# Kernel tuning notes

Hardware: AMD Instinct MI355X
Metric: run time of the kernel (lower is better)

The kernel has to match this reference:

```python
import jax, jax.numpy as jnp
import numpy as np

INF = jnp.float32(1e9)  # sentinel; true costs are O(10)


def _hungarian_cost(cost):
    """Exact min-cost perfect matching total cost (Jonker-Volgenant potentials
    algorithm, O(n^3)), matching scipy.optimize.linear_sum_assignment.
    cost: (n, n) float32 -> scalar sum of matched costs."""
    n = cost.shape[0]
    # pad with dummy row/col 0 (1-indexed algorithm)
    a = jnp.zeros((n + 1, n + 1), cost.dtype).at[1:, 1:].set(cost)

    def row_step(carry, i):
        u, v, p = carry  # u,v: dual potentials; p[j] = row matched to col j
        p = p.at[0].set(i)
        minv = jnp.full(n + 1, INF, cost.dtype)
        used = jnp.zeros(n + 1, bool)
        way = jnp.zeros(n + 1, jnp.int32)

        def cond(st):
            u, v, p, minv, used, way, j0, first = st
            return first | (p[j0] != 0)

        def body(st):
            u, v, p, minv, used, way, j0, _ = st
            used = used.at[j0].set(True)
            i0 = p[j0]
            cur = a[i0] - u[i0] - v                      # reduced costs of row i0
            upd = (~used) & (cur < minv)
            way = jnp.where(upd, j0, way)
            minv = jnp.where(upd, cur, minv)
            masked = jnp.where(used, INF, minv)
            j1 = jnp.argmin(masked).astype(jnp.int32)
            delta = masked[j1]
            # u[p[j]] += delta for used j (unused scatter adds 0, harmless)
            u = u.at[p].add(jnp.where(used, delta, 0.0))
            v = jnp.where(used, v - delta, v)
            minv = jnp.where(used, minv, minv - delta)
            return (u, v, p, minv, used, way, j1, False)

        u, v, p, minv, used, way, j0, _ = jax.lax.while_loop(
            cond, body, (u, v, p, minv, used, way, jnp.int32(0), True))

        # augment along alternating path
        def aug_body(st):
            p, j0 = st
            j1 = way[j0]
            return p.at[j0].set(p[j1]), j1

        p, _ = jax.lax.while_loop(lambda st: st[1] != 0, aug_body, (p, j0))
        return (u, v, p), None

    init = (jnp.zeros(n + 1, cost.dtype),
            jnp.zeros(n + 1, cost.dtype),
            jnp.zeros(n + 1, jnp.int32))
    (u, v, p), _ = jax.lax.scan(row_step, init,
                                jnp.arange(1, n + 1, dtype=jnp.int32))
    cols = jnp.arange(1, n + 1)
    return a[p[1:], cols].sum()


def setup_inputs() -> dict:
    key = jax.random.key(0)
    k1, k2 = jax.random.split(key)
    B, N = 8, 1024
    S1 = jax.random.normal(k1, (B, N, 3), dtype=jnp.float32)
    S2 = jax.random.normal(k2, (B, N, 3), dtype=jnp.float32)
    return {"S1": S1, "S2": S2}


def reference(S1, S2):
    B, N, _ = S1.shape
    # torch.cdist(p=2): per-sample pairwise Euclidean distances -> (B, N, N)
    diff = S1[:, :, None, :] - S2[:, None, :, :]
    cost = jnp.sqrt(jnp.sum(diff * diff, axis=-1))
    per_sample = jax.vmap(_hungarian_cost)(cost) / N  # optimal assignment cost / N
    return jnp.mean(per_sample)
```

## Files before the change

### kernel.cpp

```cpp
#include <hip/hip_runtime.h>
#include <hip/hip_fp16.h>
#include <math.h>


#define N     1024
#define BATCH 8
#define NSLOT 16
#define INFV  1e9f
#define AUC_ROUNDS 24

__global__ void emd_zero_kernel(float* out) { out[0] = 0.0f; }

__global__ __launch_bounds__(256)
void emd_dist_kernel(const float* __restrict__ S1, const float* __restrict__ S2,
                     __half* __restrict__ D) {
    int b = blockIdx.x >> 10;
    int r = blockIdx.x & (N - 1);
    const float* s1 = S1 + ((size_t)b * N + r) * 3;
    float x1 = s1[0], y1 = s1[1], z1 = s1[2];
    const float* s2 = S2 + (size_t)b * N * 3;
    __half* drow = D + ((size_t)b * N + r) * (size_t)N;
    for (int c = threadIdx.x; c < N; c += 256) {
        float dx = x1 - s2[3 * c], dy = y1 - s2[3 * c + 1], dz = z1 - s2[3 * c + 2];
        drow[c] = __float2half_rn(sqrtf(dx * dx + dy * dy + dz * dz));
    }
}

__global__ __launch_bounds__(256)
void emd_colmin_kernel(const __half* __restrict__ D, float* __restrict__ V,
                       int* __restrict__ I) {
    int b = blockIdx.x >> 2;
    int c = ((blockIdx.x & 3) << 8) + threadIdx.x;
    const __half* Db = D + ((size_t)b << 20);
    float best = INFV; int bi = 1;
    for (int r = 0; r < N; ++r) {
        float d = __half2float(Db[(size_t)r * N + c]);
        if (d < best) { best = d; bi = r + 1; }
    }
    V[b * N + c] = best;
    I[b * N + c] = bi;
}

template<int CTRL>
__device__ __forceinline__ float dppmin(float x) {
    int xi = __float_as_int(x);
    int yi = __builtin_amdgcn_update_dpp(xi, xi, CTRL, 0xF, 0xF, false);
    return fminf(x, __int_as_float(yi));
}

__device__ __forceinline__ float wave_min_f32(float x) {
    x = dppmin<0x111>(x);
    x = dppmin<0x112>(x);
    x = dppmin<0x114>(x);
    x = dppmin<0x118>(x);
    x = dppmin<0x142>(x);
    x = dppmin<0x143>(x);
    return __int_as_float(__builtin_amdgcn_readlane(__float_as_int(x), 63));
}

__global__ __launch_bounds__(1024, 1)
void emd_auction_kernel(const __half* __restrict__ Dc,
                        const float* __restrict__ Vin,
                        const int* __restrict__ Iin,
                        float* __restrict__ Vw, float* __restrict__ Uw,
                        int* __restrict__ Cw, int* __restrict__ Rw) {
    __shared__ float v0[N];
    __shared__ int   rowm[N + 1];
    __shared__ int   colm[N + 1];
    __shared__ unsigned long long bid[N + 1];
    __shared__ int   qbuf[N];
    __shared__ int   qn;

    const int tid  = threadIdx.x;
    const int lane = tid & 63;
    const int wv   = tid >> 6;
    const int b    = blockIdx.x;
    const __half* Db = Dc + ((size_t)b << 20);

    for (int t = tid; t <= N; t += 1024) { rowm[t] = 0; colm[t] = 0; bid[t] = 0ull; }
    for (int c = tid; c < N; c += 1024) v0[c] = Vin[b * N + c];
    __syncthreads();

    for (int c = tid; c < N; c += 1024) {
        int r = Iin[b * N + c];
        int old = atomicCAS(&rowm[r], 0, c + 1);
        if (old == 0) colm[c + 1] = r;
    }
    __syncthreads();

    auto rowRed16 = [&](int i, float (&red)[16]) {
        const uint4* dr = (const uint4*)(Db + (size_t)(i - 1) * N);
        uint4 w0 = dr[lane * 2 + 0];
        uint4 w1 = dr[lane * 2 + 1];
        unsigned wb[8] = { w0.x, w0.y, w0.z, w0.w, w1.x, w1.y, w1.z, w1.w };
        const float4* vp = (const float4*)(v0 + lane * 16);
        float4 vv0 = vp[0], vv1 = vp[1], vv2 = vp[2], vv3 = vp[3];
        float vv[16] = { vv0.x, vv0.y, vv0.z, vv0.w, vv1.x, vv1.y, vv1.z, vv1.w,
                         vv2.x, vv2.y, vv2.z, vv2.w, vv3.x, vv3.y, vv3.z, vv3.w };
#pragma unroll
        for (int t = 0; t < 8; ++t) {
            __half2 hh = *reinterpret_cast<const __half2*>(&wb[t]);
            float2 f2 = __half22float2(hh);
            red[2 * t]     = f2.x - vv[2 * t];
            red[2 * t + 1] = f2.y - vv[2 * t + 1];
        }
    };

    for (int round = 0; round < AUC_ROUNDS; ++round) {
        if (tid == 0) qn = 0;
        __syncthreads();
        for (int i = tid + 1; i <= N; i += 1024)
            if (rowm[i] == 0) { int p = atomicAdd(&qn, 1); qbuf[p] = i; }
        __syncthreads();
        int nq = qn;
        if (nq == 0) break;

        for (int q = wv; q < nq; q += 16) {
            int i = qbuf[q];
            float red[16];
            rowRed16(i, red);
            float a1 = INFV, a2 = INFV; int ac = 0;
            float e1 = INFV, e2 = INFV; int ec = 0;
            float f1 = INFV, f2 = INFV; int fc = 0;
            float g1 = INFV, g2 = INFV; int gc = 0;
#pragma unroll
            for (int k = 0; k < 4; ++k) {
                float u0 = red[k];
                bool t0 = u0 < a1;
                a2 = t0 ? a1 : (u0 < a2 ? u0 : a2);
                ac = t0 ? (lane * 16 + k) : ac;  a1 = t0 ? u0 : a1;
                float u1 = red[k + 4];
                bool t1 = u1 < e1;
                e2 = t1 ? e1 : (u1 < e2 ? u1 : e2);
                ec = t1 ? (lane * 16 + k + 4) : ec;  e1 = t1 ? u1 : e1;
                float u2 = red[k + 8];
                bool t2 = u2 < f1;
                f2 = t2 ? f1 : (u2 < f2 ? u2 : f2);
                fc = t2 ? (lane * 16 + k + 8) : fc;  f1 = t2 ? u2 : f1;
                float u3 = red[k + 12];
                bool t3 = u3 < g1;
                g2 = t3 ? g1 : (u3 < g2 ? u3 : g2);
                gc = t3 ? (lane * 16 + k + 12) : gc;  g1 = t3 ? u3 : g1;
            }
            bool sae = e1 < a1;
            float ae1 = sae ? e1 : a1; int aec = sae ? ec : ac;
            float ae2 = fminf(fminf(a2, e2), sae ? a1 : e1);
            bool sfg = g1 < f1;
            float fg1 = sfg ? g1 : f1; int fgc = sfg ? gc : fc;
            float fg2 = fminf(fminf(f2, g2), sfg ? f1 : g1);
            bool sall = fg1 < ae1;
            float m1 = sall ? fg1 : ae1;
            int   c1 = sall ? fgc : aec;
            float m2 = fminf(fminf(ae2, fg2), sall ? ae1 : fg1);

            float gm1 = wave_min_f32(m1);
            unsigned long long wbm = __ballot(m1 == gm1);
            int wl = __ffsll((long long)wbm) - 1;
            float cand2 = (lane == wl) ? m2 : m1;
            float gm2 = wave_min_f32(cand2);
            int gcol = __builtin_amdgcn_readlane(c1, wl);
            float inc = gm2 - gm1;

            if (lane == 0) {
                unsigned long long key =
                    ((unsigned long long)__float_as_uint(inc) << 32) |
                    (unsigned long long)(unsigned)i;
                atomicMax(&bid[gcol + 1], key);
            }
        }
        __syncthreads();

        for (int j = tid + 1; j <= N; j += 1024) {
            unsigned long long bb = bid[j];
            if (bb != 0ull) {
                bid[j] = 0ull;
                int i = (int)(unsigned)(bb & 0xFFFFFFFFull);
                float inc = __uint_as_float((unsigned)(bb >> 32));
                int old = colm[j];
                colm[j] = i;
                rowm[i] = j;
                if (old) rowm[old] = 0;
                v0[j - 1] -= inc;
            }
        }
        __syncthreads();
    }

    for (int q = wv; q < N; q += 16) {
        int i = q + 1;
        float red[16];
        rowRed16(i, red);
        int j = rowm[i];
        float rloc = red[0];
        int lo = 0, kk = 0;
        if (j) {
            lo = (j - 1) >> 4; kk = (j - 1) & 15;
#pragma unroll
            for (int k = 1; k < 16; ++k) if (k == kk) rloc = red[k];
        }
#pragma unroll
        for (int s = 1; s < 16; s <<= 1) {
#pragma unroll
            for (int k = 0; k < 16; k += 2 * s)
                red[k] = fminf(red[k], red[k + s]);
        }
        float m = wave_min_f32(red[0]);
        if (j) {
            float rm = __int_as_float(
                __builtin_amdgcn_readlane(__float_as_int(rloc), lo));
            if (lane == 0 && rm != m) { rowm[i] = 0; colm[j] = 0; }
        }
        if (lane == 0) Uw[b * N + q] = m;
    }
    __syncthreads();

    for (int c = tid; c < N; c += 1024) {
        Vw[b * N + c] = v0[c];
        Cw[b * N + c] = colm[c + 1];
    }
    for (int t = tid; t < N; t += 1024) Rw[b * N + t] = rowm[t + 1];
}

struct Frag { uint4 w0, w1; float ur; float4 q; };

template<bool CACHED, bool PRE>
__global__ __launch_bounds__(64, 1)
void emd_jv_kernel(const float* __restrict__ S1,
                   const float* __restrict__ S2,
                   const __half* __restrict__ Dc,
                   const float* __restrict__ Vin,
                   const int*   __restrict__ Iin,
                   const float* __restrict__ Uw,
                   const int*   __restrict__ Cw,
                   const int*   __restrict__ Rw,
                   float* __restrict__ out) {
    __shared__ float4 s1u[N + 1];
    __shared__ float  u_lds[N + 1];
    __shared__ float  dentry[N + 1];
    __shared__ int    rowm[N + 1];

    const int lane = threadIdx.x;
    const int b = blockIdx.x;
    const float* s1g = S1 + (size_t)b * N * 3;
    const float* s2g = S2 + (size_t)b * N * 3;
    const __half* Db = CACHED ? (Dc + ((size_t)b << 20)) : (const __half*)0;
    const float NANF = __int_as_float(0x7fc00000);

    for (int t = lane; t < N; t += 64) {
        s1u[t + 1] = make_float4(s1g[3 * t], s1g[3 * t + 1], s1g[3 * t + 2], 0.0f);
        u_lds[t + 1] = PRE ? Uw[b * N + t] : 0.0f;
        rowm[t + 1] = PRE ? Rw[b * N + t] : 0;
    }
    if (lane == 0) { u_lds[0] = 0.0f; rowm[0] = 0; }

    float v[NSLOT];
    int   pr[NSLOT];
    int   jpk[NSLOT];
    float x2[NSLOT], y2[NSLOT], z2[NSLOT];

#pragma unroll
    for (int k = 0; k < NSLOT; ++k) {
        int pt = lane * NSLOT + k;
        x2[k] = s2g[3 * pt + 0];
        y2[k] = s2g[3 * pt + 1];
        z2[k] = s2g[3 * pt + 2];
    }

    if constexpr (PRE) {
#pragma unroll
        for (int k = 0; k < NSLOT; ++k) {
            int c = lane * NSLOT + k;
            v[k] = Vin[b * N + c];
            pr[k] = Cw[b * N + c];
            jpk[k] = (pr[k] << 11) | (c + 1);
        }
        __syncthreads();
    } else {
        int imin[NSLOT];
        if constexpr (CACHED) {
#pragma unroll
            for (int k = 0; k < NSLOT; ++k) {
                int c = lane * NSLOT + k;
                v[k] = Vin[b * N + c];
                imin[k] = Iin[b * N + c];
            }
        } else {
#pragma unroll
            for (int k = 0; k < NSLOT; ++k) { v[k] = INFV; imin[k] = 1; }
        }
        __syncthreads();

        if constexpr (!CACHED) {
            for (int r = 1; r <= N; ++r) {
                float4 qq = s1u[r];
#pragma unroll
                for (int k = 0; k < NSLOT; ++k) {
                    float dx = qq.x - x2[k], dy = qq.y - y2[k], dz = qq.z - z2[k];
                    float d2 = dx * dx + dy * dy + dz * dz;
                    bool upd = d2 < v[k];
                    v[k] = upd ? d2 : v[k];
                    imin[k] = upd ? r : imin[k];
                }
            }
#pragma unroll
            for (int k = 0; k < NSLOT; ++k) v[k] = sqrtf(v[k]);
        }

#pragma unroll
        for (int k = 0; k < NSLOT; ++k) {
            int j = lane * NSLOT + k + 1;
            int r = imin[k];
            int old = atomicCAS(&rowm[r], 0, j);
            pr[k] = (old == 0) ? r : 0;
            jpk[k] = (pr[k] << 11) | j;
        }
        __syncthreads();
    }

    float minv[NSLOT];
    int   way[NSLOT];

    auto issueLoads = [&](int rr) -> Frag {
        Frag F;
        if (CACHED) {
            const uint4* dr = (const uint4*)(Db + (size_t)(rr - 1) * N);
            F.w0 = dr[lane * 2 + 0];
            F.w1 = dr[lane * 2 + 1];
        } else {
            F.q = s1u[rr];
        }
        F.ur = u_lds[rr];
        return F;
    };

    auto applyFrag = [&](const Frag& F, int jpred, float Dh) {
        float base = Dh - F.ur;
        if (CACHED) {
            float h[NSLOT];
            const unsigned* w = (const unsigned*)&F.w0;
#pragma unroll
            for (int t = 0; t < 8; ++t) {
                unsigned word = w[t];
                __half2 hh = *reinterpret_cast<const __half2*>(&word);
                float2 f2 = __half22float2(hh);
                h[2 * t] = f2.x; h[2 * t + 1] = f2.y;
            }
#pragma unroll
            for (int k = 0; k < NSLOT; ++k) {
                float cur = (h[k] - v[k]) + base;
                bool upd = cur < minv[k];
                minv[k] = upd ? cur : minv[k];
                way[k] = upd ? jpred : way[k];
            }
        } else {
#pragma unroll
            for (int k = 0; k < NSLOT; ++k) {
                float dx = F.q.x - x2[k], dy = F.q.y - y2[k], dz = F.q.z - z2[k];
                float d = sqrtf(dx * dx + dy * dy + dz * dz);
                float cur = (d - v[k]) + base;
                bool upd = cur < minv[k];
                minv[k] = upd ? cur : minv[k];
                way[k] = upd ? jpred : way[k];
            }
        }
    };

    for (int i = 1; i <= N; ++i) {
        if (rowm[i] != 0) continue;

        unsigned used = 0u;
        float DT = 0.0f;
        int freecol = 0;
        int pred = 0;
        Frag P;

        Frag F0 = issueLoads(i);
#pragma unroll
        for (int k = 0; k < NSLOT; ++k) { minv[k] = INFV; way[k] = 0; }
        applyFrag(F0, 0, 0.0f);

        int guard = 0;
        for (;;) {
            if (++guard > N + 4) break;
            float b0 = INFV, b1 = INFV, b2 = INFV, b3 = INFV;
            int   p0 = 0, p1 = 0, p2 = 0, p3 = 0;
#pragma unroll
            for (int k = 0; k < 4; ++k) {
                bool t0 = minv[k]      < b0;
                b0 = t0 ? minv[k]      : b0;  p0 = t0 ? jpk[k]      : p0;
                bool t1 = minv[k + 4]  < b1;
                b1 = t1 ? minv[k + 4]  : b1;  p1 = t1 ? jpk[k + 4]  : p1;
                bool t2 = minv[k + 8]  < b2;
                b2 = t2 ? minv[k + 8]  : b2;  p2 = t2 ? jpk[k + 8]  : p2;
                bool t3 = minv[k + 12] < b3;
                b3 = t3 ? minv[k + 12] : b3;  p3 = t3 ? jpk[k + 12] : p3;
            }
            bool m01 = b1 < b0;  float ba = m01 ? b1 : b0;  int pa = m01 ? p1 : p0;
            bool m23 = b3 < b2;  float bb = m23 ? b3 : b2;  int pb = m23 ? p3 : p2;
            bool mab = bb < ba;  float bestv = mab ? bb : ba;
            int bestjp = mab ? pb : pa;

            float gmin = wave_min_f32(bestv);
            if (!(gmin < INFV * 0.5f)) break;
            unsigned long long tm = __ballot(bestv == gmin);
            DT = gmin;
            freecol = 0;

            {
                unsigned long long tf = tm;
                while (tf) {
                    int l = __ffsll((long long)tf) - 1;
                    tf &= tf - 1;
                    int jp = __builtin_amdgcn_readlane(bestjp, l);
                    if ((jp >> 11) == 0) { freecol = jp & 0x7FF; break; }
                }
            }
            if (freecol) break;

            bool first = true;
            while (tm) {
                int l = __ffsll((long long)tm) - 1;
                tm &= tm - 1;
                int jp = __builtin_amdgcn_readlane(bestjp, l);
                int jj = jp & 0x7FF, rr = jp >> 11;
                Frag F;
                if (CACHED && first && pred != 0 && rr == pred) {
                    F = P;
                } else {
                    F = issueLoads(rr);
                }
                if (CACHED && first) {
                    float ru = (bestv == gmin) ? INFV : bestv;
                    float rmin = wave_min_f32(ru);
                    pred = 0;
                    if (rmin < INFV * 0.5f) {
                        unsigned long long rb = __ballot(ru == rmin);
                        int rl = __ffsll((long long)rb) - 1;
                        int rjp = __builtin_amdgcn_readlane(bestjp, rl);
                        int prr = rjp >> 11;
                        if (prr != 0) { pred = prr; P = issueLoads(prr); }
                    }
                }
                first = false;
                if (lane == 0) dentry[jj] = gmin;
                int cc = jj - 1, lo = cc >> 4, kk = cc & 15;
                bool mine = (lane == lo);
#pragma unroll
                for (int k = 0; k < NSLOT; ++k)
                    if (k == kk && mine) { minv[k] = NANF; used |= (1u << k); }
                applyFrag(F, jj, gmin);
            }
        }
        if (freecol == 0) continue;

        if (lane == 0) u_lds[i] += DT;
#pragma unroll
        for (int k = 0; k < NSLOT; ++k) {
            if ((used >> k) & 1u) {
                int j = lane * NSLOT + k + 1;
                float dd = DT - dentry[j];
                v[k] -= dd;
                u_lds[pr[k]] += dd;
            }
        }
        __syncthreads();

        int j0 = freecol;
        int aguard = 0;
        while (j0 != 0) {
            if (++aguard > N + 4) break;
            int cc = j0 - 1;
            int lo = cc >> 4, kk = cc & 15;
            int wloc = way[0];
#pragma unroll
            for (int k = 1; k < NSLOT; ++k) if (k == kk) wloc = way[k];
            int j1 = __builtin_amdgcn_readlane(wloc, lo);
            int np;
            if (j1 == 0) np = i;
            else {
                int c1 = j1 - 1;
                int lo1 = c1 >> 4, kk1 = c1 & 15;
                int ploc = pr[0];
#pragma unroll
                for (int k = 1; k < NSLOT; ++k) if (k == kk1) ploc = pr[k];
                np = __builtin_amdgcn_readlane(ploc, lo1);
            }
            bool mine = (lane == lo);
#pragma unroll
            for (int k = 0; k < NSLOT; ++k)
                if (k == kk) {
                    if (mine) { pr[k] = np; jpk[k] = (np << 11) | j0; }
                }
            if (lane == 0) rowm[np] = j0;
            j0 = j1;
        }
        __syncthreads();
    }

    float sum = 0.0f;
#pragma unroll
    for (int k = 0; k < NSLOT; ++k) {
        int r = pr[k] > 0 ? pr[k] : 1;
        float4 qq = s1u[r];
        float dx = qq.x - x2[k], dy = qq.y - y2[k], dz = qq.z - z2[k];
        sum += sqrtf(dx * dx + dy * dy + dz * dz);
    }
#pragma unroll
    for (int off = 32; off >= 1; off >>= 1) sum += __shfl_xor(sum, off);
    if (lane == 0) atomicAdd(out, sum * (1.0f / ((float)N * (float)BATCH)));
}

extern "C" void kernel_launch(void* const* d_in, const int* in_sizes, int n_in,
                              void* d_out, int out_size, void* d_ws, size_t ws_size,
                              hipStream_t stream) {
    const float* S1 = (const float*)d_in[0];
    const float* S2 = (const float*)d_in[1];
    float* out = (float*)d_out;

    size_t needD  = (size_t)BATCH * N * N * sizeof(__half);
    size_t vecB   = (size_t)BATCH * N * 4;
    size_t needT  = needD + 2 * vecB;
    size_t needT2 = needD + 6 * vecB;

    emd_zero_kernel<<<1, 1, 0, stream>>>(out);

    if (ws_size >= needT2) {
        __half* D  = (__half*)d_ws;
        float*  V  = (float*)((char*)d_ws + needD);
        int*    I  = (int*)((char*)V + vecB);
        float*  Vw = (float*)((char*)I + vecB);
        float*  Uw = (float*)((char*)Vw + vecB);
        int*    Cw = (int*)((char*)Uw + vecB);
        int*    Rw = (int*)((char*)Cw + vecB);
        emd_dist_kernel<<<BATCH * N, 256, 0, stream>>>(S1, S2, D);
        emd_colmin_kernel<<<BATCH * 4, 256, 0, stream>>>(D, V, I);
        emd_auction_kernel<<<BATCH, 1024, 0, stream>>>(D, V, I, Vw, Uw, Cw, Rw);
        emd_jv_kernel<true, true><<<BATCH, 64, 0, stream>>>(
            S1, S2, D, Vw, nullptr, Uw, Cw, Rw, out);
    } else if (ws_size >= needT) {
        __half* D = (__half*)d_ws;
        float*  V = (float*)((char*)d_ws + needD);
        int*    I = (int*)((char*)V + vecB);
        emd_dist_kernel<<<BATCH * N, 256, 0, stream>>>(S1, S2, D);
        emd_colmin_kernel<<<BATCH * 4, 256, 0, stream>>>(D, V, I);
        emd_jv_kernel<true, false><<<BATCH, 64, 0, stream>>>(
            S1, S2, D, V, I, nullptr, nullptr, nullptr, out);
    } else {
        emd_jv_kernel<false, false><<<BATCH, 64, 0, stream>>>(
            S1, S2, nullptr, nullptr, nullptr, nullptr, nullptr, nullptr, out);
    }
}
```

Measured before the change: 18.95 ms.

## Prefer free columns on auction ties, prefetch next tied row, double auction rounds

Raises the number of auction rounds run before the exact shortest-path phase. When the best and second-best reduced costs tie, the auction bid now goes to a currently unassigned column, so ties do not cause needless evictions. In the Dijkstra-style scan over tied minimum columns, the next row's fragment is loaded while the current one is applied, giving a software-pipelined loop. The costs are more auction work per row and extra registers for the second fragment.

```diff
diff --git a/kernel.cpp b/kernel.cpp
--- a/kernel.cpp
+++ b/kernel.cpp
@@ -7,7 +7,7 @@
 #define BATCH 8
 #define NSLOT 16
 #define INFV  1e9f
-#define AUC_ROUNDS 24
+#define AUC_ROUNDS 48
 
 __global__ void emd_zero_kernel(float* out) { out[0] = 0.0f; }
 
@@ -158,7 +158,30 @@
             int wl = __ffsll((long long)wbm) - 1;
             float cand2 = (lane == wl) ? m2 : m1;
             float gm2 = wave_min_f32(cand2);
-            int gcol = __builtin_amdgcn_readlane(c1, wl);
+            int gcol;
+            if (gm1 < gm2) {
+                gcol = __builtin_amdgcn_readlane(c1, wl);
+            } else {
+                unsigned tmask = 0u;
+#pragma unroll
+                for (int k = 0; k < 16; ++k)
+                    tmask |= (red[k] == gm1) ? (1u << k) : 0u;
+                unsigned fmask = 0u;
+                unsigned tt = tmask;
+                while (tt) {
+                    int k = __ffs((int)tt) - 1;
+                    tt &= tt - 1;
+                    if (colm[lane * 16 + k + 1] == 0) fmask |= (1u << k);
+                }
+                unsigned long long bf = __ballot(fmask != 0u);
+                if (bf != 0ull) {
+                    int l = __ffsll((long long)bf) - 1;
+                    unsigned mk = (unsigned)__builtin_amdgcn_readlane((int)fmask, l);
+                    gcol = l * 16 + (__ffs((int)mk) - 1);
+                } else {
+                    gcol = __builtin_amdgcn_readlane(c1, wl);
+                }
+            }
             float inc = gm2 - gm1;
 
             if (lane == 0) {
@@ -417,19 +440,18 @@
             }
             if (freecol) break;
 
-            bool first = true;
-            while (tm) {
-                int l = __ffsll((long long)tm) - 1;
+            {
+                int l0 = __ffsll((long long)tm) - 1;
                 tm &= tm - 1;
-                int jp = __builtin_amdgcn_readlane(bestjp, l);
-                int jj = jp & 0x7FF, rr = jp >> 11;
-                Frag F;
-                if (CACHED && first && pred != 0 && rr == pred) {
-                    F = P;
+                int jp_cur = __builtin_amdgcn_readlane(bestjp, l0);
+                int rr0 = jp_cur >> 11;
+                Frag Fcur;
+                if (CACHED && pred != 0 && rr0 == pred) {
+                    Fcur = P;
                 } else {
-                    F = issueLoads(rr);
-                }
-                if (CACHED && first) {
+                    Fcur = issueLoads(rr0);
+                }
+                if (CACHED) {
                     float ru = (bestv == gmin) ? INFV : bestv;
                     float rmin = wave_min_f32(ru);
                     pred = 0;
@@ -441,14 +463,27 @@
                         if (prr != 0) { pred = prr; P = issueLoads(prr); }
                     }
                 }
-                first = false;
-                if (lane == 0) dentry[jj] = gmin;
-                int cc = jj - 1, lo = cc >> 4, kk = cc & 15;
-                bool mine = (lane == lo);
-#pragma unroll
-                for (int k = 0; k < NSLOT; ++k)
-                    if (k == kk && mine) { minv[k] = NANF; used |= (1u << k); }
-                applyFrag(F, jj, gmin);
+                for (;;) {
+                    int jp_nxt = 0;
+                    Frag Fnxt;
+                    if (tm) {
+                        int l = __ffsll((long long)tm) - 1;
+                        tm &= tm - 1;
+                        jp_nxt = __builtin_amdgcn_readlane(bestjp, l);
+                        Fnxt = issueLoads(jp_nxt >> 11);
+                    }
+                    int jj = jp_cur & 0x7FF;
+                    if (lane == 0) dentry[jj] = gmin;
+                    int cc = jj - 1, lo = cc >> 4, kk = cc & 15;
+                    bool mine = (lane == lo);
+#pragma unroll
+                    for (int k = 0; k < NSLOT; ++k)
+                        if (k == kk && mine) { minv[k] = NANF; used |= (1u << k); }
+                    applyFrag(Fcur, jj, gmin);
+                    if (!jp_nxt) break;
+                    jp_cur = jp_nxt;
+                    Fcur = Fnxt;
+                }
             }
         }
         if (freecol == 0) continue;
```

After: 20.00 ms. +5.5%, slower.
